# Performance work log

Measured on AMD Instinct MI355X. Metric: run time of the kernel, lower is better.

Reference implementation:

```python
import jax, jax.numpy as jnp
import numpy as np

B, K, NPROP, NSAMPLE = 16, 2048, 256, 16
C_SEED, C_MLP = 256, 128
RADIUS = 0.3
NH, NSC, NCLS = 12, 18, 18
KZ, KXY, KLINE = 1024, 1024, 1024
SURF_TH, UP_TH = 0.5, 10.0
OUT_CH = 2 + 3 + 2 * NH + 4 * NSC + NCLS  # 119


def setup_inputs():
    key = jax.random.key(0)
    ks = iter(jax.random.split(key, 64))
    nrm = lambda shape, sc=1.0: sc * jax.random.normal(next(ks), shape, jnp.float32)
    uni = lambda shape: jax.random.uniform(next(ks), shape, jnp.float32, minval=-2.0, maxval=2.0)
    inp = {
        'vote_xyz': uni((B, K, 3)),
        'vote_features': nrm((B, C_SEED, K)),
        'pred_sem_class_z': nrm((B, 2, KZ)),
        'center_z': uni((B, KZ, 3)),
        'aggregated_feature_z': nrm((B, 128, KZ)),
        'pred_sem_class_xy': nrm((B, 2, KXY)),
        'center_xy': uni((B, KXY, 3)),
        'aggregated_feature_xy': nrm((B, 128, KXY)),
        'pred_sem_class_line': nrm((B, 2, KLINE)),
        'center_line': uni((B, KLINE, 3)),
        'aggregated_feature_line': nrm((B, 128, KLINE)),
        'mean_size_arr': jnp.abs(nrm((NSC, 3))) * 0.5 + 0.3,
        'mlp_w0': nrm((C_MLP, C_SEED + 3), 0.05),
        'mlp_s0': 1.0 + nrm((C_MLP,), 0.02),
        'mlp_b0': nrm((C_MLP,), 0.02),
        'mlp_w1': nrm((C_MLP, C_MLP), 0.05),
        'mlp_s1': 1.0 + nrm((C_MLP,), 0.02),
        'mlp_b1': nrm((C_MLP,), 0.02),
        'mlp_w2': nrm((C_MLP, C_MLP), 0.05),
        'mlp_s2': 1.0 + nrm((C_MLP,), 0.02),
        'mlp_b2': nrm((C_MLP,), 0.02),
        'conv1_w': nrm((C_MLP, C_MLP), 0.05),
        'conv1_b': nrm((C_MLP,), 0.02),
        'bn1_s': 1.0 + nrm((C_MLP,), 0.02),
        'bn1_b': nrm((C_MLP,), 0.02),
        'conv2_w': nrm((C_MLP, C_MLP), 0.05),
        'conv2_b': nrm((C_MLP,), 0.02),
        'bn2_s': 1.0 + nrm((C_MLP,), 0.02),
        'bn2_b': nrm((C_MLP,), 0.02),
        'conv3_w': nrm((OUT_CH, C_MLP), 0.05),
        'conv3_b': nrm((OUT_CH,), 0.02),
    }
    return inp


def fps(xyz, npoint):
    # furthest point sampling; xyz (B,N,3) -> (B,npoint) int32
    Bn, N, _ = xyz.shape
    bidx = jnp.arange(Bn)

    def step(carry, _):
        dist, far = carry
        centroid = xyz[bidx, far][:, None, :]  # (B,1,3)
        d = jnp.sum((xyz - centroid) ** 2, -1)
        dist = jnp.minimum(dist, d)
        nxt = jnp.argmax(dist, -1).astype(jnp.int32)
        return (dist, nxt), far

    init = (jnp.full((Bn, N), 1e10, xyz.dtype), jnp.zeros((Bn,), jnp.int32))
    _, inds = jax.lax.scan(step, init, None, length=npoint)
    return inds.T


def ball_group(xyz, feat_t, new_xyz, radius, nsample):
    # first-nsample-in-ball semantics (as CUDA ball_query), pad with first hit
    Bn, N, _ = xyz.shape
    d2 = jnp.sum((new_xyz[:, :, None] - xyz[:, None]) ** 2, -1)  # (B,P,N)
    score = jnp.where(d2 <= radius * radius, jnp.arange(N, dtype=jnp.int32), N)
    neg, idx = jax.lax.top_k(-score, nsample)
    idx = jnp.where(-neg < N, idx, idx[..., :1])
    b = jnp.arange(Bn)[:, None, None]
    gx = (xyz[b, idx] - new_xyz[:, :, None]) / radius  # normalize_xyz=True
    gf = feat_t[b, idx]
    return jnp.concatenate([gx, gf], -1)  # (B,P,ns,3+C)


def reference(vote_xyz, vote_features, pred_sem_class_z, center_z, aggregated_feature_z,
              pred_sem_class_xy, center_xy, aggregated_feature_xy,
              pred_sem_class_line, center_line, aggregated_feature_line, mean_size_arr,
              mlp_w0, mlp_s0, mlp_b0, mlp_w1, mlp_s1, mlp_b1, mlp_w2, mlp_s2, mlp_b2,
              conv1_w, conv1_b, bn1_s, bn1_b, conv2_w, conv2_b, bn2_s, bn2_b, conv3_w, conv3_b):
    # --- vote aggregation (PointnetSAModuleVotes, vote_fps) ---
    fps_inds = fps(vote_xyz, NPROP)
    bi = jnp.arange(vote_xyz.shape[0])[:, None]
    new_xyz = vote_xyz[bi, fps_inds]  # (B,P,3)
    g = ball_group(vote_xyz, vote_features.transpose(0, 2, 1), new_xyz, RADIUS, NSAMPLE)
    for w, s, b in ((mlp_w0, mlp_s0, mlp_b0), (mlp_w1, mlp_s1, mlp_b1), (mlp_w2, mlp_s2, mlp_b2)):
        g = jax.nn.relu(jnp.einsum('bpsc,oc->bpso', g, w) * s + b)  # conv2d 1x1 + folded BN + relu
    features = g.max(axis=2).transpose(0, 2, 1)  # (B,128,P)

    c1d = lambda x, w, b: jnp.einsum('bck,oc->bok', x, w) + b[None, :, None]
    bn = lambda x, s, b: x * s[None, :, None] + b[None, :, None]

    net = jax.nn.relu(bn(c1d(features, conv1_w, conv1_b), bn1_s, bn1_b))
    net = jax.nn.relu(bn(c1d(net, conv2_w, conv2_b), bn2_s, bn2_b))
    net = c1d(net, conv3_w, conv3_b)  # (B,119,P)

    # --- decode_scores (mode='center', start=2) ---
    nt = net.transpose(0, 2, 1)
    Bn, P = nt.shape[0], nt.shape[1]
    objectness = nt[..., 0:2]
    center = new_xyz + nt[..., 2:5]
    heading_scores = nt[..., 5:5 + NH]
    heading_res = nt[..., 5 + NH:5 + 2 * NH] * (np.pi / NH)
    size_scores = nt[..., 5 + 2 * NH:5 + 2 * NH + NSC]
    srn = nt[..., 5 + 2 * NH + NSC:5 + 2 * NH + 4 * NSC].reshape(Bn, P, NSC, 3)
    size_res = srn * mean_size_arr[None, None]
    sem_cls = nt[..., 5 + 2 * NH + 4 * NSC:]

    # --- surface / line center selection ---
    def sel_center(pred_sem, c):
        p = jax.nn.softmax(pred_sem, axis=1)
        sel = jax.lax.stop_gradient((p[:, 1, :] <= SURF_TH).astype(c.dtype))
        return c + UP_TH * sel[..., None]

    z_center = sel_center(pred_sem_class_z, center_z)
    xy_center = sel_center(pred_sem_class_xy, center_xy)
    line_center = sel_center(pred_sem_class_line, center_line)
    surface_center_pred = jnp.concatenate([z_center, xy_center], axis=1)
    surface_center_feature_pred = jnp.concatenate([aggregated_feature_z, aggregated_feature_xy], axis=2)

    # --- predicted box size -> 6 object surface centers ---
    cls = jnp.argmax(size_scores, -1)  # (B,P)
    pred_res = jnp.take_along_axis(size_res, cls[..., None, None], axis=2)[:, :, 0]
    pred_avg = mean_size_arr[cls]
    obj_size = jax.lax.stop_gradient(pred_avg + pred_res)  # .detach() in torch
    half = obj_size / 2.0
    z0 = jnp.zeros_like(half[..., :1])
    ez = jnp.concatenate([z0, z0, half[..., 2:3]], -1)
    ey = jnp.concatenate([z0, half[..., 1:2], z0], -1)
    ex = jnp.concatenate([half[..., 0:1], z0, z0], -1)
    obj_surface_center = jnp.concatenate([center + ez, center - ez, center + ey,
                                          center - ey, center + ex, center - ex], axis=1)
    obj_surface_feature = jnp.tile(features, (1, 1, 6))

    return (objectness, center, heading_scores, heading_res, size_scores, size_res, sem_cls,
            surface_center_pred, surface_center_feature_pred, line_center,
            obj_surface_center, obj_surface_feature)
```

## Files before the change

kernel.cpp:

```cpp
#include <hip/hip_runtime.h>

#define BB 16
#define KK 2048
#define NPROPN 256
#define NS 16
#define CSEED 256
#define CMLP 128
#define CIN 259
#define OUTCH 119
#define KZZ 1024

#define O0  0UL
#define O1  8192UL
#define O2  20480UL
#define O3  69632UL
#define O4  118784UL
#define O5  192512UL
#define O6  413696UL
#define O7  487424UL
#define O8  585728UL
#define O9  4780032UL
#define O10 4829184UL
#define O11 4902912UL

#define WS_NEWXYZ 0
#define WS_W0T 12288
#define WS_W1T 45440
#define WS_W2T 61824
#define WS_C1T 78208
#define WS_C2T 94592
#define WS_C3T 110976
#define WS_FEATT 131072UL
#define WS_NEED_BYTES ((size_t)(WS_FEATT + (size_t)BB * KK * CSEED) * 4)

#define XROWS 131
#define XSTR (XROWS * 16)

#define RSTEP(CTRL)                                                                          \
  {                                                                                          \
    unsigned shi = (unsigned)__builtin_amdgcn_update_dpp((int)hi, (int)hi, (CTRL), 0xF, 0xF, false); \
    unsigned slo = (unsigned)__builtin_amdgcn_update_dpp((int)lo, (int)lo, (CTRL), 0xF, 0xF, false); \
    bool gt = (shi > hi) || ((shi == hi) && (slo > lo));                                     \
    hi = gt ? shi : hi;                                                                      \
    lo = gt ? slo : lo;                                                                      \
  }

__device__ __forceinline__ void fma4(float4& a, float s, const float4& w) {
  a.x = fmaf(s, w.x, a.x); a.y = fmaf(s, w.y, a.y);
  a.z = fmaf(s, w.z, a.z); a.w = fmaf(s, w.w, a.w);
}
__device__ __forceinline__ float fget(const float4& v, int r) {
  return r == 0 ? v.x : (r == 1 ? v.y : (r == 2 ? v.z : v.w));
}
__device__ __forceinline__ int xadr(int row, int s4) {
  return row * 16 + (((s4) ^ ((row >> 2) & 3)) << 2);
}

template<bool TR>
__global__ __launch_bounds__(256) void prep_kernel(
    const float* __restrict__ xyz, const float* __restrict__ vote_feat,
    const float* __restrict__ w0, const float* __restrict__ w1, const float* __restrict__ w2,
    const float* __restrict__ c1w, const float* __restrict__ c2w, const float* __restrict__ c3w,
    const float* __restrict__ pz, const float* __restrict__ cz,
    const float* __restrict__ pxy, const float* __restrict__ cxy,
    const float* __restrict__ pl, const float* __restrict__ cl,
    const float* __restrict__ az, const float* __restrict__ axy,
    float* __restrict__ wsf, float* __restrict__ out) {
  constexpr int FPS_END = 16;
  constexpr int FEATT_END = FPS_END + (TR ? 1024 : 0);
  constexpr int TRW_END = FEATT_END + 450;
  constexpr int SURF_END = TRW_END + 192;

  const int bid = blockIdx.x;
  const int t = threadIdx.x;
  __shared__ float smem[8448];
  __shared__ float wvv[2][4];
  __shared__ int wii[2][4];

  if (bid < FPS_END) {
    const int b = bid;
    const float* p = xyz + (size_t)b * KK * 3;
    float* sxyz = smem;
    float* nxb = smem + 6144;
    const int lane = t & 63, w = t >> 6;
    float pxr[8], pyr[8], pzr[8], dd[8];
#pragma unroll
    for (int j = 0; j < 8; ++j) {
      int i = j * 256 + t;
      float x = p[i * 3 + 0], y = p[i * 3 + 1], z = p[i * 3 + 2];
      pxr[j] = x; pyr[j] = y; pzr[j] = z; dd[j] = 1e10f;
      sxyz[i * 3 + 0] = x; sxyz[i * 3 + 1] = y; sxyz[i * 3 + 2] = z;
    }
    __syncthreads();
    int cur = 0;
    for (int it = 0; it < NPROPN; ++it) {
      const int pb = it & 1;
      float cx = sxyz[cur * 3 + 0];
      float cy = sxyz[cur * 3 + 1];
      float cz2 = sxyz[cur * 3 + 2];
      if (t == 0) { nxb[it * 3 + 0] = cx; nxb[it * 3 + 1] = cy; nxb[it * 3 + 2] = cz2; }
      float best = -1.0f;
      int bidx = 0;
#pragma unroll
      for (int j = 0; j < 8; ++j) {
        float dx = __fsub_rn(pxr[j], cx);
        float dy = __fsub_rn(pyr[j], cy);
        float dz = __fsub_rn(pzr[j], cz2);
        float d = __fadd_rn(__fadd_rn(__fmul_rn(dx, dx), __fmul_rn(dy, dy)), __fmul_rn(dz, dz));
        float nd = fminf(dd[j], d);
        dd[j] = nd;
        if (nd > best) { best = nd; bidx = j * 256 + t; }
      }
      unsigned hi = __float_as_uint(best);
      unsigned lo = ~(unsigned)bidx;
      RSTEP(0x111) RSTEP(0x112) RSTEP(0x114) RSTEP(0x118)
      RSTEP(0x142) RSTEP(0x143)
      if (lane == 63) { wvv[pb][w] = __uint_as_float(hi); wii[pb][w] = (int)lo; }
      __syncthreads();
      unsigned vh = __float_as_uint(wvv[pb][0]);
      unsigned vl = (unsigned)wii[pb][0];
#pragma unroll
      for (int q2 = 1; q2 < 4; ++q2) {
        unsigned ah = __float_as_uint(wvv[pb][q2]);
        unsigned al = (unsigned)wii[pb][q2];
        bool gt = (ah > vh) || ((ah == vh) && (al > vl));
        vh = gt ? ah : vh; vl = gt ? al : vl;
      }
      cur = (int)~vl;
    }
    __syncthreads();
    float* nxw = wsf + WS_NEWXYZ + (size_t)b * NPROPN * 3;
    for (int i = t; i < NPROPN * 3; i += 256) nxw[i] = nxb[i];
    return;
  }

  if (TR && bid < FEATT_END) {
    int q = bid - FPS_END;
    int b = q >> 6, ck = q & 63;
    int k0 = ck << 5;
    float* tile = smem;
    const float* src = vote_feat + ((size_t)b * CSEED + t) * KK + k0;
    float4 v[8];
#pragma unroll
    for (int j = 0; j < 8; ++j) v[j] = *(const float4*)(src + j * 4);
#pragma unroll
    for (int j = 0; j < 8; ++j) {
      tile[(j * 4 + 0) * 260 + t] = v[j].x;
      tile[(j * 4 + 1) * 260 + t] = v[j].y;
      tile[(j * 4 + 2) * 260 + t] = v[j].z;
      tile[(j * 4 + 3) * 260 + t] = v[j].w;
    }
    __syncthreads();
    float* dst = wsf + WS_FEATT + ((size_t)b * KK + k0) * CSEED;
    const int kk = t >> 3, cbase = (t & 7) << 2;
#pragma unroll
    for (int j = 0; j < 8; ++j) {
      int c = cbase + (j << 5);
      float4 u = make_float4(tile[kk * 260 + c], tile[kk * 260 + c + 1],
                             tile[kk * 260 + c + 2], tile[kk * 260 + c + 3]);
      *(float4*)(dst + (size_t)kk * CSEED + c) = u;
    }
    return;
  }

  if (bid < TRW_END) {
    int row = (bid - FEATT_END) * 2 + (t >> 7);
    int o = t & 127;
    if (row < 899) {
      float v; float* dst;
      if (row < 259)      { dst = wsf + WS_W0T + (size_t)row * 128; v = w0[(size_t)o * CIN + row]; }
      else if (row < 387) { int k = row - 259; dst = wsf + WS_W1T + (size_t)k * 128; v = w1[(size_t)o * 128 + k]; }
      else if (row < 515) { int k = row - 387; dst = wsf + WS_W2T + (size_t)k * 128; v = w2[(size_t)o * 128 + k]; }
      else if (row < 643) { int k = row - 515; dst = wsf + WS_C1T + (size_t)k * 128; v = c1w[(size_t)o * 128 + k]; }
      else if (row < 771) { int k = row - 643; dst = wsf + WS_C2T + (size_t)k * 128; v = c2w[(size_t)o * 128 + k]; }
      else                { int k = row - 771; dst = wsf + WS_C3T + (size_t)k * 128; v = (o < OUTCH) ? c3w[(size_t)o * 128 + k] : 0.f; }
      dst[o] = v;
    }
    return;
  }

  if (bid < SURF_END) {
    int i = (bid - TRW_END) * 256 + t;
    int src = i / (BB * KZZ);
    int rem = i % (BB * KZZ);
    int b = rem / KZZ, k = rem % KZZ;
    const float* ps = (src == 0) ? pz : ((src == 1) ? pxy : pl);
    const float* pc = (src == 0) ? cz : ((src == 1) ? cxy : cl);
    float x0 = ps[((size_t)b * 2 + 0) * KZZ + k];
    float x1 = ps[((size_t)b * 2 + 1) * KZZ + k];
    float add = (x1 <= x0) ? 10.0f : 0.0f;
    size_t dst;
    if (src == 0)      dst = O7 + ((size_t)b * 2048 + k) * 3;
    else if (src == 1) dst = O7 + ((size_t)b * 2048 + 1024 + k) * 3;
    else               dst = O9 + ((size_t)b * KZZ + k) * 3;
    const float* c3 = pc + ((size_t)b * KZZ + k) * 3;
    out[dst + 0] = c3[0] + add;
    out[dst + 1] = c3[1] + add;
    out[dst + 2] = c3[2] + add;
    return;
  }

  {
    int i = (bid - SURF_END) * 256 + t;
    int q = i & 511;
    int bc = i >> 9;
    int half = q >> 8, k4 = q & 255;
    const float4* src = (const float4*)((half == 0) ? az : axy);
    float4 v = src[(size_t)bc * 256 + k4];
    float4* dst = (float4*)(out + O8);
    dst[(size_t)bc * 512 + q] = v;
  }
}

__device__ __forceinline__ void mlp_accum(const float* __restrict__ WT, int og, int sh,
                                          const float* __restrict__ xb, int K, float4* acc) {
  const float4* wp = (const float4*)WT + og;
  const int s4a = sh * 2, s4b = sh * 2 + 1;
#pragma unroll 4
  for (int k = 0; k < K; ++k) {
    float4 xa = *(const float4*)(xb + xadr(k, s4a));
    float4 xq = *(const float4*)(xb + xadr(k, s4b));
    float4 wv = wp[(size_t)k * 32];
    fma4(acc[0], xa.x, wv); fma4(acc[1], xa.y, wv);
    fma4(acc[2], xa.z, wv); fma4(acc[3], xa.w, wv);
    fma4(acc[4], xq.x, wv); fma4(acc[5], xq.y, wv);
    fma4(acc[6], xq.z, wv); fma4(acc[7], xq.w, wv);
  }
}

__device__ __forceinline__ void mlp_accum_pair(const float* __restrict__ WT, int og, int sh,
                                               const float* __restrict__ xb, int K, float4* acc) {
  const float4* wp = (const float4*)WT + og;
#pragma unroll 4
  for (int k2 = 0; k2 < K; k2 += 2) {
    int myk = k2 + sh;
    int mk = myk < K ? myk : (K - 1);
    float4 xa = *(const float4*)(xb + xadr(mk, 0));
    float4 xq = *(const float4*)(xb + xadr(mk, 1));
    float4 wv = wp[(size_t)mk * 32];
    if (myk < K) {
      fma4(acc[0], xa.x, wv); fma4(acc[1], xa.y, wv);
      fma4(acc[2], xa.z, wv); fma4(acc[3], xa.w, wv);
      fma4(acc[4], xq.x, wv); fma4(acc[5], xq.y, wv);
      fma4(acc[6], xq.z, wv); fma4(acc[7], xq.w, wv);
    }
  }
}

__device__ __forceinline__ void pair_combine(float4* acc) {
#pragma unroll
  for (int i = 0; i < 8; ++i) {
    acc[i].x += __shfl_xor(acc[i].x, 32);
    acc[i].y += __shfl_xor(acc[i].y, 32);
    acc[i].z += __shfl_xor(acc[i].z, 32);
    acc[i].w += __shfl_xor(acc[i].w, 32);
  }
}

__device__ __forceinline__ void mlp_storeh(const float* __restrict__ scv, const float* __restrict__ bbv,
                                           int og, int sh, float* __restrict__ xb,
                                           const float4* __restrict__ acc) {
  float4 s4v = *(const float4*)(scv + (og << 2));
  float4 b4v = *(const float4*)(bbv + (og << 2));
#pragma unroll
  for (int r = 0; r < 4; ++r) {
    float ss = fget(s4v, r), bv = fget(b4v, r);
    float4 lo, hi;
    lo.x = fmaf(fget(acc[0], r), ss, bv); lo.x = lo.x > 0.f ? lo.x : 0.f;
    lo.y = fmaf(fget(acc[1], r), ss, bv); lo.y = lo.y > 0.f ? lo.y : 0.f;
    lo.z = fmaf(fget(acc[2], r), ss, bv); lo.z = lo.z > 0.f ? lo.z : 0.f;
    lo.w = fmaf(fget(acc[3], r), ss, bv); lo.w = lo.w > 0.f ? lo.w : 0.f;
    hi.x = fmaf(fget(acc[4], r), ss, bv); hi.x = hi.x > 0.f ? hi.x : 0.f;
    hi.y = fmaf(fget(acc[5], r), ss, bv); hi.y = hi.y > 0.f ? hi.y : 0.f;
    hi.z = fmaf(fget(acc[6], r), ss, bv); hi.z = hi.z > 0.f ? hi.z : 0.f;
    hi.w = fmaf(fget(acc[7], r), ss, bv); hi.w = hi.w > 0.f ? hi.w : 0.f;
    int row = (og << 2) + r;
    *(float4*)(xb + xadr(row, sh * 2)) = lo;
    *(float4*)(xb + xadr(row, sh * 2 + 1)) = hi;
  }
}

__device__ __forceinline__ float4 conv_accum(const float* __restrict__ CT,
                                             const float* __restrict__ xp,
                                             int og, int sh) {
  float4 a = make_float4(0.f, 0.f, 0.f, 0.f);
  const float4* wp = (const float4*)CT + og;
#pragma unroll 8
  for (int j = 0; j < 64; ++j) {
    int k = (j << 1) + sh;
    float f = xp[k];
    float4 wv = wp[(size_t)k * 32];
    a.x = fmaf(f, wv.x, a.x);
    a.y = fmaf(f, wv.y, a.y);
    a.z = fmaf(f, wv.z, a.z);
    a.w = fmaf(f, wv.w, a.w);
  }
  a.x += __shfl_xor(a.x, 32);
  a.y += __shfl_xor(a.y, 32);
  a.z += __shfl_xor(a.z, 32);
  a.w += __shfl_xor(a.w, 32);
  return a;
}

template<bool TR>
__global__ __launch_bounds__(256, 4) void proposal_kernel(
    const float* __restrict__ vote_xyz, const float* __restrict__ vote_feat,
    const float* __restrict__ wsf, const float* __restrict__ msa,
    const float* __restrict__ s0, const float* __restrict__ b0,
    const float* __restrict__ s1, const float* __restrict__ b1,
    const float* __restrict__ s2, const float* __restrict__ b2,
    const float* __restrict__ c1b, const float* __restrict__ bn1s, const float* __restrict__ bn1b,
    const float* __restrict__ c2b, const float* __restrict__ bn2s, const float* __restrict__ bn2b,
    const float* __restrict__ c3b,
    float* __restrict__ out) {
  __shared__ __align__(16) float Xbuf[4 * XSTR];
  __shared__ int sel_s[4][NS];
  __shared__ float sc_s[4][3], sh_s[4][3];
  __shared__ int scls_s[4];

  const int t = threadIdx.x;
  const int w = t >> 6, l = t & 63;
  const int b = blockIdx.x >> 6;
  const int pp = ((blockIdx.x & 63) << 2) + w;
  const int sh = l >> 5, og = l & 31;
  float* Xw = Xbuf + w * XSTR;
  float* feat_p = Xw;
  float* n1_p   = Xw + 128;
  float* n2_p   = Xw + 256;
  float* ntv_p  = Xw + 384;

  const float* nx = wsf + WS_NEWXYZ + ((size_t)b * NPROPN + pp) * 3;
  const float cx = nx[0], cy = nx[1], cz = nx[2];
  const float* px = vote_xyz + (size_t)b * KK * 3;
  const float RR = 0.09000000357627869f;

  int total = 0;
  {
    for (int j0 = 0; j0 < 32 && total < NS; j0 += 8) {
      float dq[8];
#pragma unroll
      for (int jj = 0; jj < 8; ++jj) {
        int i = ((j0 + jj) << 6) + l;
        float dx = __fsub_rn(px[i * 3 + 0], cx);
        float dy = __fsub_rn(px[i * 3 + 1], cy);
        float dz = __fsub_rn(px[i * 3 + 2], cz);
        dq[jj] = __fadd_rn(__fadd_rn(__fmul_rn(dx, dx), __fmul_rn(dy, dy)), __fmul_rn(dz, dz));
      }
#pragma unroll
      for (int jj = 0; jj < 8; ++jj) {
        bool in = (dq[jj] <= RR);
        unsigned long long bal = __ballot(in);
        if (in) {
          int pos = total + __popcll(bal & ((1ull << l) - 1ull));
          if (pos < NS) sel_s[w][pos] = ((j0 + jj) << 6) + l;
        }
        total += __popcll(bal);
      }
    }
    if (l == 0 && total < NS) {
      int first = (total > 0) ? sel_s[w][0] : 0;
      for (int i = total; i < NS; ++i) sel_s[w][i] = first;
    }
    __builtin_amdgcn_wave_barrier();
  }

  float4 pf[8];
  {
    const int s = l >> 2, q = l & 3;
    const int idx = sel_s[w][s];
    const int s4 = s >> 2, se = s & 3;
    if (q < 3) {
      float pv = px[idx * 3 + q];
      float cv = (q == 0) ? cx : ((q == 1) ? cy : cz);
      Xw[xadr(q, s4) + se] = __fdiv_rn(__fsub_rn(pv, cv), 0.3f);
    }
    if constexpr (TR) {
      const float* fr = wsf + WS_FEATT + ((size_t)b * KK + idx) * CSEED;
#pragma unroll
      for (int m = 0; m < 8; ++m) {
        int c = (m << 4) + (q << 2);
        float4 v = *(const float4*)(fr + c);
        Xw[xadr(3 + c + 0, s4) + se] = v.x;
        Xw[xadr(3 + c + 1, s4) + se] = v.y;
        Xw[xadr(3 + c + 2, s4) + se] = v.z;
        Xw[xadr(3 + c + 3, s4) + se] = v.w;
      }
#pragma unroll
      for (int m = 0; m < 8; ++m) pf[m] = *(const float4*)(fr + 128 + (m << 4) + (q << 2));
    } else {
      const float* fb = vote_feat + (size_t)b * CSEED * KK + idx;
#pragma unroll
      for (int m = 0; m < 8; ++m) {
        int c = (m << 4) + (q << 2);
        Xw[xadr(3 + c + 0, s4) + se] = fb[(size_t)(c + 0) * KK];
        Xw[xadr(3 + c + 1, s4) + se] = fb[(size_t)(c + 1) * KK];
        Xw[xadr(3 + c + 2, s4) + se] = fb[(size_t)(c + 2) * KK];
        Xw[xadr(3 + c + 3, s4) + se] = fb[(size_t)(c + 3) * KK];
      }
#pragma unroll
      for (int m = 0; m < 8; ++m) {
        int c = 128 + (m << 4) + (q << 2);
        pf[m].x = fb[(size_t)(c + 0) * KK];
        pf[m].y = fb[(size_t)(c + 1) * KK];
        pf[m].z = fb[(size_t)(c + 2) * KK];
        pf[m].w = fb[(size_t)(c + 3) * KK];
      }
    }
    __builtin_amdgcn_wave_barrier();
  }

  auto write_chunk1 = [&]() {
    const int s = l >> 2, q = l & 3;
    const int s4 = s >> 2, se = s & 3;
#pragma unroll
    for (int m = 0; m < 8; ++m) {
      int c = (m << 4) + (q << 2);
      Xw[xadr(c + 0, s4) + se] = pf[m].x;
      Xw[xadr(c + 1, s4) + se] = pf[m].y;
      Xw[xadr(c + 2, s4) + se] = pf[m].z;
      Xw[xadr(c + 3, s4) + se] = pf[m].w;
    }
  };

  float4 acc[8];
#pragma unroll
  for (int i = 0; i < 8; ++i) acc[i] = make_float4(0.f, 0.f, 0.f, 0.f);

  if (total <= 8) {
    mlp_accum_pair(wsf + WS_W0T, og, sh, Xw, 131, acc);
    __builtin_amdgcn_wave_barrier();
    write_chunk1();
    __builtin_amdgcn_wave_barrier();
    mlp_accum_pair(wsf + WS_W0T + 131 * 128, og, sh, Xw, 128, acc);
    pair_combine(acc);
    mlp_storeh(s0, b0, og, sh, Xw, acc);
    __builtin_amdgcn_wave_barrier();
#pragma unroll
    for (int i = 0; i < 8; ++i) acc[i] = make_float4(0.f, 0.f, 0.f, 0.f);
    mlp_accum_pair(wsf + WS_W1T, og, sh, Xw, 128, acc);
    pair_combine(acc);
    mlp_storeh(s1, b1, og, sh, Xw, acc);
    __builtin_amdgcn_wave_barrier();
#pragma unroll
    for (int i = 0; i < 8; ++i) acc[i] = make_float4(0.f, 0.f, 0.f, 0.f);
    mlp_accum_pair(wsf + WS_W2T, og, sh, Xw, 128, acc);
    pair_combine(acc);
  } else {
    mlp_accum(wsf + WS_W0T, og, sh, Xw, 131, acc);
    __builtin_amdgcn_wave_barrier();
    write_chunk1();
    __builtin_amdgcn_wave_barrier();
    mlp_accum(wsf + WS_W0T + 131 * 128, og, sh, Xw, 128, acc);
    mlp_storeh(s0, b0, og, sh, Xw, acc);
    __builtin_amdgcn_wave_barrier();
#pragma unroll
    for (int i = 0; i < 8; ++i) acc[i] = make_float4(0.f, 0.f, 0.f, 0.f);
    mlp_accum(wsf + WS_W1T, og, sh, Xw, 128, acc);
    mlp_storeh(s1, b1, og, sh, Xw, acc);
    __builtin_amdgcn_wave_barrier();
#pragma unroll
    for (int i = 0; i < 8; ++i) acc[i] = make_float4(0.f, 0.f, 0.f, 0.f);
    mlp_accum(wsf + WS_W2T, og, sh, Xw, 128, acc);
  }

  float mr[4];
  {
    float4 s4v = *(const float4*)(s2 + (og << 2));
    float4 b4v = *(const float4*)(b2 + (og << 2));
#pragma unroll
    for (int r = 0; r < 4; ++r) {
      float ss = fget(s4v, r), bv = fget(b4v, r);
      float m = 0.f;
#pragma unroll
      for (int i = 0; i < 8; ++i) m = fmaxf(m, fmaf(fget(acc[i], r), ss, bv));
      mr[r] = fmaxf(m, __shfl_xor(m, 32));
    }
  }
  __builtin_amdgcn_wave_barrier();
  if (sh == 0) *(float4*)(feat_p + (og << 2)) = make_float4(mr[0], mr[1], mr[2], mr[3]);
  __builtin_amdgcn_wave_barrier();

  {
    float* o11 = out + O11 + (size_t)b * CMLP * 1536;
#pragma unroll
    for (int r = 0; r < 4; ++r) {
      size_t rowb = (size_t)((og << 2) + r) * 1536 + pp;
#pragma unroll
      for (int rr2 = 0; rr2 < 3; ++rr2) {
        int rr = sh * 3 + rr2;
        o11[rowb + rr * 256] = mr[r];
      }
    }
  }

  {
    float4 a = conv_accum(wsf + WS_C1T, feat_p, og, sh);
    int o = og << 2;
    float4 res;
    res.x = fmaf(a.x + c1b[o + 0], bn1s[o + 0], bn1b[o + 0]); res.x = res.x > 0.f ? res.x : 0.f;
    res.y = fmaf(a.y + c1b[o + 1], bn1s[o + 1], bn1b[o + 1]); res.y = res.y > 0.f ? res.y : 0.f;
    res.z = fmaf(a.z + c1b[o + 2], bn1s[o + 2], bn1b[o + 2]); res.z = res.z > 0.f ? res.z : 0.f;
    res.w = fmaf(a.w + c1b[o + 3], bn1s[o + 3], bn1b[o + 3]); res.w = res.w > 0.f ? res.w : 0.f;
    if (sh == 0) *(float4*)(n1_p + o) = res;
    __builtin_amdgcn_wave_barrier();
  }
  {
    float4 a = conv_accum(wsf + WS_C2T, n1_p, og, sh);
    int o = og << 2;
    float4 res;
    res.x = fmaf(a.x + c2b[o + 0], bn2s[o + 0], bn2b[o + 0]); res.x = res.x > 0.f ? res.x : 0.f;
    res.y = fmaf(a.y + c2b[o + 1], bn2s[o + 1], bn2b[o + 1]); res.y = res.y > 0.f ? res.y : 0.f;
    res.z = fmaf(a.z + c2b[o + 2], bn2s[o + 2], bn2b[o + 2]); res.z = res.z > 0.f ? res.z : 0.f;
    res.w = fmaf(a.w + c2b[o + 3], bn2s[o + 3], bn2b[o + 3]); res.w = res.w > 0.f ? res.w : 0.f;
    if (sh == 0) *(float4*)(n2_p + o) = res;
    __builtin_amdgcn_wave_barrier();
  }
  {
    float4 a = conv_accum(wsf + WS_C3T, n2_p, og, sh);
    int o = og << 2;
    float4 res;
    res.x = a.x + ((o + 0 < OUTCH) ? c3b[o + 0] : 0.f);
    res.y = a.y + ((o + 1 < OUTCH) ? c3b[o + 1] : 0.f);
    res.z = a.z + ((o + 2 < OUTCH) ? c3b[o + 2] : 0.f);
    res.w = a.w + ((o + 3 < OUTCH) ? c3b[o + 3] : 0.f);
    if (sh == 0 && o < 120) *(float4*)(ntv_p + o) = res;
    __builtin_amdgcn_wave_barrier();
  }

  {
    const size_t bp = (size_t)b * NPROPN + pp;
    if (l < 2) out[O0 + bp * 2 + l] = ntv_p[l];
    if (l < 3) {
      float cv = ((l == 0) ? cx : ((l == 1) ? cy : cz)) + ntv_p[2 + l];
      sc_s[w][l] = cv;
      out[O1 + bp * 3 + l] = cv;
    }
    if (l < 12) {
      out[O2 + bp * 12 + l] = ntv_p[5 + l];
      out[O3 + bp * 12 + l] = ntv_p[17 + l] * 0.2617993877991494f;
    }
    if (l < 18) {
      out[O4 + bp * 18 + l] = ntv_p[29 + l];
      out[O6 + bp * 18 + l] = ntv_p[101 + l];
    }
    if (l < 54) out[O5 + bp * 54 + l] = ntv_p[47 + l] * msa[l];
    if (l == 0) {
      float bvv = ntv_p[29]; int bii = 0;
      for (int i2 = 1; i2 < 18; ++i2)
        if (ntv_p[29 + i2] > bvv) { bvv = ntv_p[29 + i2]; bii = i2; }
      scls_s[w] = bii;
    }
    __builtin_amdgcn_wave_barrier();
    if (l < 3) {
      int cls = scls_s[w];
      float m = msa[cls * 3 + l];
      sh_s[w][l] = fmaf(ntv_p[47 + cls * 3 + l], m, m) * 0.5f;
    }
    __builtin_amdgcn_wave_barrier();
    if (l < 18) {
      const int r = l / 3, j2 = l % 3;
      const int axis[6] = {2, 2, 1, 1, 0, 0};
      float v = sc_s[w][j2];
      if (j2 == axis[r]) v = (r & 1) ? (v - sh_s[w][j2]) : (v + sh_s[w][j2]);
      out[O10 + (size_t)b * 4608 + (size_t)(r * 256 + pp) * 3 + j2] = v;
    }
  }
}

extern "C" void kernel_launch(void* const* d_in, const int* in_sizes, int n_in,
                              void* d_out, int out_size, void* d_ws, size_t ws_size,
                              hipStream_t stream) {
  (void)in_sizes; (void)n_in; (void)out_size;
  const float* vote_xyz = (const float*)d_in[0];
  const float* vote_feat = (const float*)d_in[1];
  const float* pz   = (const float*)d_in[2];
  const float* cz   = (const float*)d_in[3];
  const float* az   = (const float*)d_in[4];
  const float* pxy  = (const float*)d_in[5];
  const float* cxy  = (const float*)d_in[6];
  const float* axy  = (const float*)d_in[7];
  const float* pl   = (const float*)d_in[8];
  const float* cl   = (const float*)d_in[9];
  const float* msa  = (const float*)d_in[11];
  const float* w0   = (const float*)d_in[12];
  const float* s0   = (const float*)d_in[13];
  const float* b0   = (const float*)d_in[14];
  const float* w1   = (const float*)d_in[15];
  const float* s1   = (const float*)d_in[16];
  const float* b1   = (const float*)d_in[17];
  const float* w2   = (const float*)d_in[18];
  const float* s2   = (const float*)d_in[19];
  const float* b2   = (const float*)d_in[20];
  const float* c1w  = (const float*)d_in[21];
  const float* c1b  = (const float*)d_in[22];
  const float* bn1s = (const float*)d_in[23];
  const float* bn1b = (const float*)d_in[24];
  const float* c2w  = (const float*)d_in[25];
  const float* c2b  = (const float*)d_in[26];
  const float* bn2s = (const float*)d_in[27];
  const float* bn2b = (const float*)d_in[28];
  const float* c3w  = (const float*)d_in[29];
  const float* c3b  = (const float*)d_in[30];
  float* out = (float*)d_out;
  float* wsf = (float*)d_ws;

  if (ws_size >= WS_NEED_BYTES) {
    hipLaunchKernelGGL((prep_kernel<true>), dim3(16 + 1024 + 450 + 192 + 4096), dim3(256), 0, stream,
                       vote_xyz, vote_feat, w0, w1, w2, c1w, c2w, c3w,
                       pz, cz, pxy, cxy, pl, cl, az, axy, wsf, out);
    hipLaunchKernelGGL((proposal_kernel<true>), dim3(BB * NPROPN / 4), dim3(256), 0, stream,
                       vote_xyz, vote_feat, wsf, msa,
                       s0, b0, s1, b1, s2, b2,
                       c1b, bn1s, bn1b, c2b, bn2s, bn2b, c3b, out);
  } else {
    hipLaunchKernelGGL((prep_kernel<false>), dim3(16 + 450 + 192 + 4096), dim3(256), 0, stream,
                       vote_xyz, vote_feat, w0, w1, w2, c1w, c2w, c3w,
                       pz, cz, pxy, cxy, pl, cl, az, axy, wsf, out);
    hipLaunchKernelGGL((proposal_kernel<false>), dim3(BB * NPROPN / 4), dim3(256), 0, stream,
                       vote_xyz, vote_feat, wsf, msa,
                       s0, b0, s1, b1, s2, b2,
                       c1b, bn1s, bn1b, c2b, bn2s, bn2b, c3b, out);
  }
}
```

Baseline: 310.6 us.

## Process grouped samples in 8-wide passes to halve LDS and raise occupancy

The per-wave shared-memory activation tile now holds 8 samples instead of 16, so the shared-MLP runs once for the first 8 grouped samples and, when more than 8 neighbours are found, runs a second time on the remaining 8. The max-pool result is accumulated across the passes. The old 16-wide path is removed and launch bounds go from 4 to 8 blocks per CU, which cuts LDS and register footprint to allow more waves per CU. In exchange, the weights are streamed twice whenever a group has more than 8 samples, and the pair-combine shuffles are now always executed.

```diff
diff --git a/kernel.cpp b/kernel.cpp
--- a/kernel.cpp
+++ b/kernel.cpp
@@ -34,7 +34,7 @@
 #define WS_NEED_BYTES ((size_t)(WS_FEATT + (size_t)BB * KK * CSEED) * 4)
 
 #define XROWS 131
-#define XSTR (XROWS * 16)
+#define XSTR8 (XROWS * 8 + 8)
 
 #define RSTEP(CTRL)                                                                          \
   {                                                                                          \
@@ -52,8 +52,8 @@
 __device__ __forceinline__ float fget(const float4& v, int r) {
   return r == 0 ? v.x : (r == 1 ? v.y : (r == 2 ? v.z : v.w));
 }
-__device__ __forceinline__ int xadr(int row, int s4) {
-  return row * 16 + (((s4) ^ ((row >> 2) & 3)) << 2);
+__device__ __forceinline__ int xadr8(int row, int s4) {
+  return row * 8 + (((s4) ^ (row & 1)) << 2);
 }
 
 template<bool TR>
@@ -212,31 +212,15 @@
   }
 }
 
-__device__ __forceinline__ void mlp_accum(const float* __restrict__ WT, int og, int sh,
-                                          const float* __restrict__ xb, int K, float4* acc) {
-  const float4* wp = (const float4*)WT + og;
-  const int s4a = sh * 2, s4b = sh * 2 + 1;
-#pragma unroll 4
-  for (int k = 0; k < K; ++k) {
-    float4 xa = *(const float4*)(xb + xadr(k, s4a));
-    float4 xq = *(const float4*)(xb + xadr(k, s4b));
-    float4 wv = wp[(size_t)k * 32];
-    fma4(acc[0], xa.x, wv); fma4(acc[1], xa.y, wv);
-    fma4(acc[2], xa.z, wv); fma4(acc[3], xa.w, wv);
-    fma4(acc[4], xq.x, wv); fma4(acc[5], xq.y, wv);
-    fma4(acc[6], xq.z, wv); fma4(acc[7], xq.w, wv);
-  }
-}
-
-__device__ __forceinline__ void mlp_accum_pair(const float* __restrict__ WT, int og, int sh,
-                                               const float* __restrict__ xb, int K, float4* acc) {
+__device__ __forceinline__ void mlp_accum8(const float* __restrict__ WT, int og, int sh,
+                                           const float* __restrict__ xb, int K, float4* acc) {
   const float4* wp = (const float4*)WT + og;
 #pragma unroll 4
   for (int k2 = 0; k2 < K; k2 += 2) {
     int myk = k2 + sh;
     int mk = myk < K ? myk : (K - 1);
-    float4 xa = *(const float4*)(xb + xadr(mk, 0));
-    float4 xq = *(const float4*)(xb + xadr(mk, 1));
+    float4 xa = *(const float4*)(xb + xadr8(mk, 0));
+    float4 xq = *(const float4*)(xb + xadr8(mk, 1));
     float4 wv = wp[(size_t)mk * 32];
     if (myk < K) {
       fma4(acc[0], xa.x, wv); fma4(acc[1], xa.y, wv);
@@ -257,26 +241,21 @@
   }
 }
 
-__device__ __forceinline__ void mlp_storeh(const float* __restrict__ scv, const float* __restrict__ bbv,
-                                           int og, int sh, float* __restrict__ xb,
-                                           const float4* __restrict__ acc) {
+__device__ __forceinline__ void mlp_storeh8(const float* __restrict__ scv, const float* __restrict__ bbv,
+                                            int og, int sh, float* __restrict__ xb,
+                                            const float4* __restrict__ acc) {
   float4 s4v = *(const float4*)(scv + (og << 2));
   float4 b4v = *(const float4*)(bbv + (og << 2));
+  const float4* a = acc + (sh << 2);
 #pragma unroll
   for (int r = 0; r < 4; ++r) {
     float ss = fget(s4v, r), bv = fget(b4v, r);
-    float4 lo, hi;
-    lo.x = fmaf(fget(acc[0], r), ss, bv); lo.x = lo.x > 0.f ? lo.x : 0.f;
-    lo.y = fmaf(fget(acc[1], r), ss, bv); lo.y = lo.y > 0.f ? lo.y : 0.f;
-    lo.z = fmaf(fget(acc[2], r), ss, bv); lo.z = lo.z > 0.f ? lo.z : 0.f;
-    lo.w = fmaf(fget(acc[3], r), ss, bv); lo.w = lo.w > 0.f ? lo.w : 0.f;
-    hi.x = fmaf(fget(acc[4], r), ss, bv); hi.x = hi.x > 0.f ? hi.x : 0.f;
-    hi.y = fmaf(fget(acc[5], r), ss, bv); hi.y = hi.y > 0.f ? hi.y : 0.f;
-    hi.z = fmaf(fget(acc[6], r), ss, bv); hi.z = hi.z > 0.f ? hi.z : 0.f;
-    hi.w = fmaf(fget(acc[7], r), ss, bv); hi.w = hi.w > 0.f ? hi.w : 0.f;
-    int row = (og << 2) + r;
-    *(float4*)(xb + xadr(row, sh * 2)) = lo;
-    *(float4*)(xb + xadr(row, sh * 2 + 1)) = hi;
+    float4 h;
+    h.x = fmaf(fget(a[0], r), ss, bv); h.x = h.x > 0.f ? h.x : 0.f;
+    h.y = fmaf(fget(a[1], r), ss, bv); h.y = h.y > 0.f ? h.y : 0.f;
+    h.z = fmaf(fget(a[2], r), ss, bv); h.z = h.z > 0.f ? h.z : 0.f;
+    h.w = fmaf(fget(a[3], r), ss, bv); h.w = h.w > 0.f ? h.w : 0.f;
+    *(float4*)(xb + xadr8((og << 2) + r, sh)) = h;
   }
 }
 
@@ -303,7 +282,7 @@
 }
 
 template<bool TR>
-__global__ __launch_bounds__(256, 4) void proposal_kernel(
+__global__ __launch_bounds__(256, 8) void proposal_kernel(
     const float* __restrict__ vote_xyz, const float* __restrict__ vote_feat,
     const float* __restrict__ wsf, const float* __restrict__ msa,
     const float* __restrict__ s0, const float* __restrict__ b0,
@@ -313,7 +292,7 @@
     const float* __restrict__ c2b, const float* __restrict__ bn2s, const float* __restrict__ bn2b,
     const float* __restrict__ c3b,
     float* __restrict__ out) {
-  __shared__ __align__(16) float Xbuf[4 * XSTR];
+  __shared__ __align__(16) float Xbuf[4 * XSTR8];
   __shared__ int sel_s[4][NS];
   __shared__ float sc_s[4][3], sh_s[4][3];
   __shared__ int scls_s[4];
@@ -323,7 +302,7 @@
   const int b = blockIdx.x >> 6;
   const int pp = ((blockIdx.x & 63) << 2) + w;
   const int sh = l >> 5, og = l & 31;
-  float* Xw = Xbuf + w * XSTR;
+  float* Xw = Xbuf + w * XSTR8;
   float* feat_p = Xw;
   float* n1_p   = Xw + 128;
   float* n2_p   = Xw + 256;
@@ -364,118 +343,112 @@
     __builtin_amdgcn_wave_barrier();
   }
 
-  float4 pf[8];
-  {
-    const int s = l >> 2, q = l & 3;
-    const int idx = sel_s[w][s];
+  float4 pf[4];
+  auto gather8 = [&](int base) {
+    const int s = l >> 3, q = l & 7;
+    const int idx = sel_s[w][base + s];
     const int s4 = s >> 2, se = s & 3;
     if (q < 3) {
       float pv = px[idx * 3 + q];
       float cv = (q == 0) ? cx : ((q == 1) ? cy : cz);
-      Xw[xadr(q, s4) + se] = __fdiv_rn(__fsub_rn(pv, cv), 0.3f);
+      Xw[xadr8(q, s4) + se] = __fdiv_rn(__fsub_rn(pv, cv), 0.3f);
     }
     if constexpr (TR) {
       const float* fr = wsf + WS_FEATT + ((size_t)b * KK + idx) * CSEED;
 #pragma unroll
-      for (int m = 0; m < 8; ++m) {
-        int c = (m << 4) + (q << 2);
+      for (int m = 0; m < 4; ++m) {
+        int c = (m << 5) + (q << 2);
         float4 v = *(const float4*)(fr + c);
-        Xw[xadr(3 + c + 0, s4) + se] = v.x;
-        Xw[xadr(3 + c + 1, s4) + se] = v.y;
-        Xw[xadr(3 + c + 2, s4) + se] = v.z;
-        Xw[xadr(3 + c + 3, s4) + se] = v.w;
-      }
-#pragma unroll
-      for (int m = 0; m < 8; ++m) pf[m] = *(const float4*)(fr + 128 + (m << 4) + (q << 2));
+        Xw[xadr8(3 + c + 0, s4) + se] = v.x;
+        Xw[xadr8(3 + c + 1, s4) + se] = v.y;
+        Xw[xadr8(3 + c + 2, s4) + se] = v.z;
+        Xw[xadr8(3 + c + 3, s4) + se] = v.w;
+      }
+#pragma unroll
+      for (int m = 0; m < 4; ++m) pf[m] = *(const float4*)(fr + 128 + (m << 5) + (q << 2));
     } else {
       const float* fb = vote_feat + (size_t)b * CSEED * KK + idx;
 #pragma unroll
-      for (int m = 0; m < 8; ++m) {
-        int c = (m << 4) + (q << 2);
-        Xw[xadr(3 + c + 0, s4) + se] = fb[(size_t)(c + 0) * KK];
-        Xw[xadr(3 + c + 1, s4) + se] = fb[(size_t)(c + 1) * KK];
-        Xw[xadr(3 + c + 2, s4) + se] = fb[(size_t)(c + 2) * KK];
-        Xw[xadr(3 + c + 3, s4) + se] = fb[(size_t)(c + 3) * KK];
-      }
-#pragma unroll
-      for (int m = 0; m < 8; ++m) {
-        int c = 128 + (m << 4) + (q << 2);
+      for (int m = 0; m < 4; ++m) {
+        int c = (m << 5) + (q << 2);
+        Xw[xadr8(3 + c + 0, s4) + se] = fb[(size_t)(c + 0) * KK];
+        Xw[xadr8(3 + c + 1, s4) + se] = fb[(size_t)(c + 1) * KK];
+        Xw[xadr8(3 + c + 2, s4) + se] = fb[(size_t)(c + 2) * KK];
+        Xw[xadr8(3 + c + 3, s4) + se] = fb[(size_t)(c + 3) * KK];
+      }
+#pragma unroll
+      for (int m = 0; m < 4; ++m) {
+        int c = 128 + (m << 5) + (q << 2);
         pf[m].x = fb[(size_t)(c + 0) * KK];
         pf[m].y = fb[(size_t)(c + 1) * KK];
         pf[m].z = fb[(size_t)(c + 2) * KK];
         pf[m].w = fb[(size_t)(c + 3) * KK];
       }
     }
-    __builtin_amdgcn_wave_barrier();
-  }
-
+  };
   auto write_chunk1 = [&]() {
-    const int s = l >> 2, q = l & 3;
+    const int s = l >> 3, q = l & 7;
     const int s4 = s >> 2, se = s & 3;
 #pragma unroll
-    for (int m = 0; m < 8; ++m) {
-      int c = (m << 4) + (q << 2);
-      Xw[xadr(c + 0, s4) + se] = pf[m].x;
-      Xw[xadr(c + 1, s4) + se] = pf[m].y;
-      Xw[xadr(c + 2, s4) + se] = pf[m].z;
-      Xw[xadr(c + 3, s4) + se] = pf[m].w;
+    for (int m = 0; m < 4; ++m) {
+      int c = (m << 5) + (q << 2);
+      Xw[xadr8(c + 0, s4) + se] = pf[m].x;
+      Xw[xadr8(c + 1, s4) + se] = pf[m].y;
+      Xw[xadr8(c + 2, s4) + se] = pf[m].z;
+      Xw[xadr8(c + 3, s4) + se] = pf[m].w;
     }
   };
 
   float4 acc[8];
-#pragma unroll
-  for (int i = 0; i < 8; ++i) acc[i] = make_float4(0.f, 0.f, 0.f, 0.f);
-
-  if (total <= 8) {
-    mlp_accum_pair(wsf + WS_W0T, og, sh, Xw, 131, acc);
+  auto run_mlp8 = [&]() {
+#pragma unroll
+    for (int i = 0; i < 8; ++i) acc[i] = make_float4(0.f, 0.f, 0.f, 0.f);
+    mlp_accum8(wsf + WS_W0T, og, sh, Xw, 131, acc);
     __builtin_amdgcn_wave_barrier();
     write_chunk1();
     __builtin_amdgcn_wave_barrier();
-    mlp_accum_pair(wsf + WS_W0T + 131 * 128, og, sh, Xw, 128, acc);
+    mlp_accum8(wsf + WS_W0T + 131 * 128, og, sh, Xw, 128, acc);
     pair_combine(acc);
-    mlp_storeh(s0, b0, og, sh, Xw, acc);
+    mlp_storeh8(s0, b0, og, sh, Xw, acc);
     __builtin_amdgcn_wave_barrier();
 #pragma unroll
     for (int i = 0; i < 8; ++i) acc[i] = make_float4(0.f, 0.f, 0.f, 0.f);
-    mlp_accum_pair(wsf + WS_W1T, og, sh, Xw, 128, acc);
+    mlp_accum8(wsf + WS_W1T, og, sh, Xw, 128, acc);
     pair_combine(acc);
-    mlp_storeh(s1, b1, og, sh, Xw, acc);
+    mlp_storeh8(s1, b1, og, sh, Xw, acc);
     __builtin_amdgcn_wave_barrier();
 #pragma unroll
     for (int i = 0; i < 8; ++i) acc[i] = make_float4(0.f, 0.f, 0.f, 0.f);
-    mlp_accum_pair(wsf + WS_W2T, og, sh, Xw, 128, acc);
+    mlp_accum8(wsf + WS_W2T, og, sh, Xw, 128, acc);
     pair_combine(acc);
-  } else {
-    mlp_accum(wsf + WS_W0T, og, sh, Xw, 131, acc);
-    __builtin_amdgcn_wave_barrier();
-    write_chunk1();
-    __builtin_amdgcn_wave_barrier();
-    mlp_accum(wsf + WS_W0T + 131 * 128, og, sh, Xw, 128, acc);
-    mlp_storeh(s0, b0, og, sh, Xw, acc);
-    __builtin_amdgcn_wave_barrier();
-#pragma unroll
-    for (int i = 0; i < 8; ++i) acc[i] = make_float4(0.f, 0.f, 0.f, 0.f);
-    mlp_accum(wsf + WS_W1T, og, sh, Xw, 128, acc);
-    mlp_storeh(s1, b1, og, sh, Xw, acc);
-    __builtin_amdgcn_wave_barrier();
-#pragma unroll
-    for (int i = 0; i < 8; ++i) acc[i] = make_float4(0.f, 0.f, 0.f, 0.f);
-    mlp_accum(wsf + WS_W2T, og, sh, Xw, 128, acc);
-  }
-
-  float mr[4];
-  {
+  };
+
+  float mr[4] = {0.f, 0.f, 0.f, 0.f};
+  auto maxpool8 = [&]() {
     float4 s4v = *(const float4*)(s2 + (og << 2));
     float4 b4v = *(const float4*)(b2 + (og << 2));
 #pragma unroll
     for (int r = 0; r < 4; ++r) {
       float ss = fget(s4v, r), bv = fget(b4v, r);
-      float m = 0.f;
+      float m = mr[r];
 #pragma unroll
       for (int i = 0; i < 8; ++i) m = fmaxf(m, fmaf(fget(acc[i], r), ss, bv));
-      mr[r] = fmaxf(m, __shfl_xor(m, 32));
-    }
-  }
+      mr[r] = m;
+    }
+  };
+
+  gather8(0);
+  __builtin_amdgcn_wave_barrier();
+  run_mlp8();
+  maxpool8();
+  if (total > 8) {
+    __builtin_amdgcn_wave_barrier();
+    gather8(8);
+    __builtin_amdgcn_wave_barrier();
+    run_mlp8();
+    maxpool8();
+  }
+
   __builtin_amdgcn_wave_barrier();
   if (sh == 0) *(float4*)(feat_p + (og << 2)) = make_float4(mr[0], mr[1], mr[2], mr[3]);
   __builtin_amdgcn_wave_barrier();
```

Result: slower. 958.5 us (+208.6%).
